# Performance work log

Measured on AMD Instinct MI355X. Metric: run time of the kernel, lower is better.

## Reference

```python
import jax, jax.numpy as jnp
import numpy as np
from jax import lax

D_INNER = 1024
D_STATE = 16
DT_RANK = 32


def conv2d(x, w, b, pad=1):
    y = lax.conv_general_dilated(x, w, (1, 1), [(pad, pad), (pad, pad)],
                                 dimension_numbers=('NCHW', 'OIHW', 'NCHW'))
    return y + b[None, :, None, None]


def maxpool2(x):
    return lax.reduce_window(x, -jnp.inf, lax.max, (1, 1, 2, 2), (1, 1, 2, 2), 'VALID')


def layer_norm(x, w, b, eps=1e-5):
    m = x.mean(-1, keepdims=True)
    v = ((x - m) ** 2).mean(-1, keepdims=True)
    return (x - m) * lax.rsqrt(v + eps) * w + b


def cblock(h, w1, b1, w2, b2):
    return jax.nn.relu(conv2d(jax.nn.relu(conv2d(h, w1, b1)), w2, b2))


def up2(d, w, b):
    # ConvTranspose2d(kernel=2, stride=2): each input pixel -> 2x2 output block
    Bn, Ci, H, W = d.shape
    y = jnp.einsum('bcij,copq->boipjq', d, w).reshape(Bn, w.shape[1], 2 * H, 2 * W)
    return y + b[None, :, None, None]


def eblock(e, d, upw, upb, w1, b1, w2, b2):
    d = up2(d, upw, upb)
    dy = e.shape[2] - d.shape[2]
    dx = e.shape[3] - d.shape[3]
    e = e[:, :, dy // 2:e.shape[2] - dy // 2, dx // 2:e.shape[3] - dx // 2]
    return cblock(jnp.concatenate([e, d], 1), w1, b1, w2, b2)


def mamba(hs, inW, cw, cb, xpW, dtW, dtB, Alog, Dp, outW):
    # standard Mamba-1 mixer: in_proj -> causal depthwise conv -> selective scan -> gate -> out_proj
    Bn, L, _ = hs.shape
    xz = jnp.einsum('bld,ed->ble', hs, inW)                       # [B,L,2*d_inner]
    xi, z = xz[..., :D_INNER], xz[..., D_INNER:]
    xc = lax.conv_general_dilated(xi.transpose(0, 2, 1), cw[:, None, :], (1,), [(3, 0)],
                                  dimension_numbers=('NCH', 'OIH', 'NCH'),
                                  feature_group_count=D_INNER)    # causal, len L
    xc = jax.nn.silu(xc + cb[None, :, None]).transpose(0, 2, 1)   # [B,L,d_inner]
    xdbl = jnp.einsum('bld,ed->ble', xc, xpW)                     # [B,L,dt_rank+2*d_state]
    dt = jax.nn.softplus(jnp.einsum('blr,dr->bld', xdbl[..., :DT_RANK], dtW) + dtB)
    Bs = xdbl[..., DT_RANK:DT_RANK + D_STATE]
    Cs = xdbl[..., DT_RANK + D_STATE:]
    A = -jnp.exp(Alog)                                            # [d_inner,d_state]
    dA = jnp.exp(dt[..., None] * A)                               # [B,L,d_inner,d_state]
    dBu = (dt * xc)[..., None] * Bs[:, :, None, :]

    def step(h, inp):
        dA_t, dBu_t, C_t = inp
        h = dA_t * h + dBu_t
        return h, jnp.einsum('bdn,bn->bd', h, C_t)

    h0 = jnp.zeros((Bn, D_INNER, D_STATE), hs.dtype)
    _, ys = lax.scan(step, h0, (dA.transpose(1, 0, 2, 3), dBu.transpose(1, 0, 2, 3), Cs.transpose(1, 0, 2)))
    y = ys.transpose(1, 0, 2) + Dp * xc
    return jnp.einsum('ble,de->bld', y * jax.nn.silu(z), outW)


def setup_inputs() -> dict:
    key = jax.random.key(0)
    ks = iter(jax.random.split(key, 80))

    def w(shape, fan_in):
        return jax.random.normal(next(ks), shape, jnp.float32) * np.float32(np.sqrt(2.0 / fan_in))

    H = W = 128
    fy = np.fft.fftfreq(H)
    fx = np.fft.fftfreq(W)
    r = np.sqrt(fy[:, None] ** 2 + fx[None, :] ** 2)
    r = r / r.max()
    bands = [(0.0, 0.15), (0.15, 0.35), (0.35, 1.0001)]
    freq_masks = jnp.asarray(np.stack([((r >= lo) & (r < hi)).astype(np.float32) for lo, hi in bands]))

    d = {}
    d['x'] = jax.random.normal(next(ks), (2, 1, H, W), jnp.float32)
    d['freq_masks'] = freq_masks
    for ci, co, n in [(3, 64, 'e1'), (64, 128, 'e2'), (128, 256, 'e3'), (256, 512, 'e4')]:
        d[n + 'w1'] = w((co, ci, 3, 3), ci * 9)
        d[n + 'b1'] = jnp.zeros((co,), jnp.float32)
        d[n + 'w2'] = w((co, co, 3, 3), co * 9)
        d[n + 'b2'] = jnp.zeros((co,), jnp.float32)
    d['cls_token'] = jnp.zeros((1, 1, 512), jnp.float32)
    d['norm_w'] = jnp.ones((24, 512), jnp.float32)
    d['norm_b'] = jnp.zeros((24, 512), jnp.float32)
    d['in_proj_w'] = w((24, 2048, 512), 512)
    d['conv1d_w'] = w((24, 1024, 4), 4)
    d['conv1d_b'] = jnp.zeros((24, 1024), jnp.float32)
    d['x_proj_w'] = w((24, 64, 1024), 1024)
    d['dt_w'] = w((24, 1024, 32), 32)
    d['dt_b'] = jnp.full((24, 1024), float(np.log(np.expm1(0.01))), jnp.float32)
    d['A_log'] = jnp.broadcast_to(jnp.log(jnp.arange(1, 17, dtype=jnp.float32)), (24, 1024, 16)) + 0.0
    d['D_ssm'] = jnp.ones((24, 1024), jnp.float32)
    d['out_proj_w'] = w((24, 512, 1024), 1024)
    for n, ci, co, cc in [('d4', 512, 256, 768), ('d3', 256, 128, 384), ('d2', 128, 64, 192), ('d1', 64, 32, 96)]:
        d[n + 'up_w'] = w((ci, co, 2, 2), ci * 4)
        d[n + 'up_b'] = jnp.zeros((co,), jnp.float32)
        d[n + 'w1'] = w((co, cc, 3, 3), cc * 9)
        d[n + 'b1'] = jnp.zeros((co,), jnp.float32)
        d[n + 'w2'] = w((co, co, 3, 3), co * 9)
        d[n + 'b2'] = jnp.zeros((co,), jnp.float32)
    d['final_w'] = w((4, 32, 1, 1), 32)
    d['final_b'] = jnp.zeros((4,), jnp.float32)
    return d


def reference(x, freq_masks, e1w1, e1b1, e1w2, e1b2, e2w1, e2b1, e2w2, e2b2,
              e3w1, e3b1, e3w2, e3b2, e4w1, e4b1, e4w2, e4b2, cls_token,
              norm_w, norm_b, in_proj_w, conv1d_w, conv1d_b, x_proj_w, dt_w, dt_b,
              A_log, D_ssm, out_proj_w,
              d4up_w, d4up_b, d4w1, d4b1, d4w2, d4b2,
              d3up_w, d3up_b, d3w1, d3b1, d3w2, d3b2,
              d2up_w, d2up_b, d2w1, d2b1, d2w2, d2b2,
              d1up_w, d1up_b, d1w1, d1b1, d1w2, d1b2,
              final_w, final_b):
    # DCT/FFT frequency split: [B,1,H,W] -> [B,3,H,W]
    xf = jnp.fft.fft2(x)
    x_freq = jnp.real(jnp.fft.ifft2(xf * freq_masks[None]))

    e1 = cblock(x_freq, e1w1, e1b1, e1w2, e1b2); p1 = maxpool2(e1)
    e2 = cblock(p1, e2w1, e2b1, e2w2, e2b2); p2 = maxpool2(e2)
    e3 = cblock(p2, e3w1, e3b1, e3w2, e3b2); p3 = maxpool2(e3)
    e4 = cblock(p3, e4w1, e4b1, e4w2, e4b2); p4 = maxpool2(e4)   # [B,512,H/16,W/16]

    Bn, _, Hs, Ws = p4.shape
    seq = p4.reshape(Bn, 512, Hs * Ws).transpose(0, 2, 1)
    tok = jnp.concatenate([jnp.broadcast_to(cls_token, (Bn, 1, 512)), seq], 1)

    params = (norm_w, norm_b, in_proj_w, conv1d_w, conv1d_b, x_proj_w, dt_w, dt_b, A_log, D_ssm, out_proj_w)

    def layer(carry, p):
        hidden, residual = carry
        nw, nb, inW, cw, cb, xpW, dtW, dtB, Alog, Dp, outW = p
        residual = residual + hidden   # first block: residual starts == hidden (faithful)
        hs = layer_norm(residual, nw, nb)
        hs = mamba(hs, inW, cw, cb, xpW, dtW, dtB, Alog, Dp, outW)
        return (hs, residual), None

    (hidden, _), _ = lax.scan(layer, (tok, tok), params)

    xsp = hidden[:, 1:, :].transpose(0, 2, 1).reshape(Bn, 512, Hs, Ws)

    d4 = eblock(e4, xsp, d4up_w, d4up_b, d4w1, d4b1, d4w2, d4b2)
    d3 = eblock(e3, d4, d3up_w, d3up_b, d3w1, d3b1, d3w2, d3b2)
    d2 = eblock(e2, d3, d2up_w, d2up_b, d2w1, d2b1, d2w2, d2b2)
    d1 = eblock(e1, d2, d1up_w, d1up_b, d1w1, d1b1, d1w2, d1b2)

    out = conv2d(d1, final_w, final_b, pad=0)
    out = jax.image.resize(out, (out.shape[0], out.shape[1], out.shape[2] * 16, out.shape[3] * 16), 'bilinear')
    return out
```

## Files before the change

kernel.cpp:

```cpp
#include <hip/hip_runtime.h>
#include <math.h>

#define PI_F 3.14159265358979323846f
typedef _Float16 f16;
typedef __attribute__((ext_vector_type(8))) _Float16 f16x8;
typedef __attribute__((ext_vector_type(4))) float f32x4;

__device__ __forceinline__ float siluf(float x){ return x / (1.f + expf(-x)); }
__device__ __forceinline__ float softplusf(float x){ return fmaxf(x,0.f) + log1pf(expf(-fabsf(x))); }
__device__ __forceinline__ void f2hl(float v, f16& hi, f16& lo){
  hi = (f16)v;
  lo = (f16)(v - (float)hi);
}

__global__ void k_dft_rows(const float* __restrict__ x, float* __restrict__ Tre, float* __restrict__ Tim){
  int v = threadIdx.x; int y = blockIdx.x; int b = blockIdx.y;
  __shared__ float cs[128], sn[128];
  float ang = -2.f*PI_F*(float)v/128.f;
  cs[v]=cosf(ang); sn[v]=sinf(ang);
  __syncthreads();
  const float* row = x + (b*128+y)*128;
  float re=0.f, im=0.f;
  for(int n=0;n<128;n++){ float xv=row[n]; int ph=(v*n)&127; re=fmaf(xv,cs[ph],re); im=fmaf(xv,sn[ph],im); }
  int o=(b*128+y)*128+v; Tre[o]=re; Tim[o]=im;
// ... 45 lines not shown
  }
  xf[((b*3+m)*128+y)*128+xc] = re*(1.f/128.f);
}

#define NWD 20
struct WAll {
  const float* src[NWD];
  int N[NWD], Kp[NWD], up[NWD], ci[NWD], cip[NWD];
  int cum[NWD+1];
};
__global__ void k_wcvt_all(WAll d, int total, f16* __restrict__ bh, f16* __restrict__ bl){
  int gid = blockIdx.x*256 + threadIdx.x;
  if (gid >= total) return;
  int li = gid; const float* src = d.src[0];
  int N=d.N[0], Kp=d.Kp[0], up=d.up[0], Ci=d.ci[0], cip=d.cip[0];
  #pragma unroll
  for (int j=1;j<NWD;j++){
    if (gid >= d.cum[j]){
      li = gid - d.cum[j]; src=d.src[j]; N=d.N[j];Kp=d.Kp[j];up=d.up[j];Ci=d.ci[j];cip=d.cip[j];
    }
  }
  int n = li / Kp, k = li - n*Kp;
  float v = 0.f;
  if (up){
    int o = n>>2, p=(n>>1)&1, q=n&1;
    if (k < Ci) v = src[(((size_t)k*up + o)*2 + p)*2 + q];
  } else {
    int tap = k / cip, cc = k - tap*cip;
    if (n < N && cc < Ci) v = src[((size_t)n*Ci + cc)*9 + tap];
  }
  f16 h,l; f2hl(v,h,l);
  bh[gid]=h; bl[gid]=l;
}

__global__ void k_im2col(const float* __restrict__ in1, int C1,
                         int H, int W, int wsh, int hwsh, int K, int Kp,
                         f16* __restrict__ Ah, f16* __restrict__ Al){
  int k = blockIdx.x*256 + threadIdx.x;
  int lm = blockIdx.y;
  if (k >= Kp) return;
  float val = 0.f;
  if (k < K){
    int m = lm;
    int b = m >> hwsh;
    int hw = m & ((1<<hwsh)-1);
    int y = hw >> wsh;
    int x = hw & (W-1);
    val = in1[(((size_t)b*C1 + k)*H + y)*W + x];
  }
  f16 h,l; f2hl(val,h,l);
  Ah[(size_t)lm*Kp + k] = h; Al[(size_t)lm*Kp + k] = l;
}

#define GLLDS(gp, ls) __builtin_amdgcn_global_load_lds( \
    (const __attribute__((address_space(1))) void*)(gp), \
    (__attribute__((address_space(3))) void*)(ls), 16, 0, 0)

template<int NL>
__global__ __launch_bounds__(256) void k_conv_ig(
    const float* __restrict__ in1, int C1, const float* __restrict__ in2, int C2,
    const f16* __restrict__ Wh, const f16* __restrict__ Wl,
    const float* __restrict__ bias, float* __restrict__ out,
    int Co, int H, int W, int wsh, int hwsh, int Cip, int civ,
    int nslabR, float* __restrict__ part, int Np)
{
  __shared__ __align__(16) float smI[2*6464];
  __shared__ __align__(16) f16 smW[3*2*2048];
  const int HW = 1<<hwsh;
  const int tw = (W<64)?W:64;
  const int twsh = (wsh<6)?wsh:6;
  const int R = 64>>twsh;
  const int RT = R+2, TWD = tw+2;
  const int nspat = RT*TWD;
  const int CS = ((nspat+3)&~3)+2;
  const int total = nspat*32;
  const int nsteps = 9*nslabR;
  const int Kp = 9*Cip;
  int slab0 = blockIdx.z*nslabR;
  int slabEnd = slab0 + nslabR;

  int bn = blockIdx.y*64;
  int bm = blockIdx.x*64;
  int t = threadIdx.x;
  int lane = t&63, wv = t>>6;
  int wr = wv>>1, wc = wv&1;

  int b  = bm >> hwsh;
  int hw0 = bm & (HW-1);
  int y0 = hw0 >> wsh;
  int x0 = hw0 & (W-1);

  float bv[2][4];
  if (!part){
    int cb = bn + wr*32 + (lane>>4)*4;
    #pragma unroll
    for (int ri=0;ri<2;ri++)
      #pragma unroll
      for (int r=0;r<4;r++){
        int co = cb + ri*16 + r;
        bv[ri][r] = bias[co < Co ? co : Co-1];
      }
    asm volatile("s_waitcnt vmcnt(0)" ::: "memory");
  }

  int goff[NL], loff[NL];
  {
    int ci = 0, s = t;
    if (s >= nspat){ s -= nspat; ci++; }
    if (s >= nspat){ s -= nspat; ci++; }
    #pragma unroll
    for (int j=0;j<NL;j++){
      int rr_=0, sx=s;
      #pragma unroll
      for (int q=0;q<5;q++){ if (sx>=TWD){ sx-=TWD; rr_++; } }
      int gy = y0 - 1 + rr_;
      int gx = x0 - 1 + sx;
      int idx = t + j*256;
      bool intile = (idx < total);
      bool ok = intile && (ci < civ) && (gy>=0) && (gy<H) && (gx>=0) && (gx<W);
      goff[j] = ok ? (ci*HW + gy*W + gx) : -1;
      loff[j] = intile ? (ci*CS + rr_*TWD + sx) : -1;
      s += 256;
      if (s >= nspat){ s -= nspat; ci++; }
      if (s >= nspat){ s -= nspat; ci++; }
      if (s >= nspat){ s -= nspat; ci++; }
    }
  }

  int rr = lane >> 2;
  int cg = (lane & 3) ^ ((lane >> 3) & 3);
  size_t gW = (size_t)(bn + wv*16 + rr)*Kp + cg*8;
  int lb = wv*512;
  auto stage = [&](int bfi, int k0){
    GLLDS(Wh + gW + k0, &smW[(bfi*2+0)*2048 + lb]);
    GLLDS(Wl + gW + k0, &smW[(bfi*2+1)*2048 + lb]);
  };

  int rA = lane & 15, c = lane >> 4;
  int RW = wr*32 + rA; int sW = (RW>>1)&3;
  int offW = RW*32 + 8*(c ^ sW);
  int lp0 = wc*32 + rA, lp1 = lp0 + 16;
  int sid0 = ((lp0>>twsh)+1)*TWD + (lp0 & (tw-1)) + 1;
  int sid1 = ((lp1>>twsh)+1)*TWD + (lp1 & (tw-1)) + 1;
  int cbase = c*8*CS;
  int csj[8];
  #pragma unroll
  for (int j=0;j<8;j++) csj[j] = j*CS;

  auto srcptr = [&](int sl) -> const float* {
    int cbeg = sl*32;
    return (cbeg < C1) ? in1 + ((size_t)(b*C1 + cbeg))*HW
                       : in2 + ((size_t)(b*C2 + (cbeg - C1)))*HW;
  };

  float rin[NL];
  {
    const float* sp = srcptr(slab0);
    #pragma unroll
    for (int j=0;j<NL;j++) rin[j] = sp[goff[j] < 0 ? 0 : goff[j]];
  }
  stage(0, 0*Cip + slab0*32);
  stage(1, 1*Cip + slab0*32);
  stage(2, 2*Cip + slab0*32);
  asm volatile("s_waitcnt vmcnt(6)" ::: "memory");
  #pragma unroll
  for (int j=0;j<NL;j++) if (loff[j] >= 0) smI[loff[j]] = (goff[j] < 0) ? 0.f : rin[j];
  asm volatile("s_waitcnt lgkmcnt(0)" ::: "memory");
  __builtin_amdgcn_s_barrier();
  asm volatile("" ::: "memory");
  if (slab0 + 1 < slabEnd){
    const float* sp = srcptr(slab0+1);
    #pragma unroll
    for (int j=0;j<NL;j++) rin[j] = sp[goff[j] < 0 ? 0 : goff[j]];
  }

  f32x4 zz = {0.f,0.f,0.f,0.f};
  f32x4 acc[2][2];
  acc[0][0]=zz; acc[0][1]=zz; acc[1][0]=zz; acc[1][1]=zz;

  int tcur = 0, scur = slab0;
  int stp_t3 = 3, stp_s3 = slab0;
  int bfi = 0;

  for (int step = 0; step < nsteps; ++step){
    if (tcur == 0 && step > 0){
      asm volatile("s_waitcnt vmcnt(6)" ::: "memory");
      int wb = ((scur - slab0) & 1)*6464;
      #pragma unroll
      for (int j=0;j<NL;j++) if (loff[j] >= 0) smI[wb + loff[j]] = (goff[j] < 0) ? 0.f : rin[j];
      asm volatile("s_waitcnt lgkmcnt(0)" ::: "memory");
      __builtin_amdgcn_s_barrier();
      asm volatile("" ::: "memory");
      if (scur + 1 < slabEnd){
        const float* sp = srcptr(scur+1);
        #pragma unroll
        for (int j=0;j<NL;j++) rin[j] = sp[goff[j] < 0 ? 0 : goff[j]];
      }
    }
    if (tcur < 3 && (scur + 1 < slabEnd)){
      if constexpr (NL == 25) asm volatile("s_waitcnt vmcnt(29)" ::: "memory");
      else if constexpr (NL == 17) asm volatile("s_waitcnt vmcnt(21)" ::: "memory");
      else asm volatile("s_waitcnt vmcnt(18)" ::: "memory");
    } else {
      asm volatile("s_waitcnt vmcnt(4)" ::: "memory");
    }
    __builtin_amdgcn_s_barrier();
    asm volatile("" ::: "memory");

    const f16* bW = &smW[bfi*4096];
    f16x8 w0h = *(const f16x8*)&bW[offW];
    f16x8 w1h = *(const f16x8*)&bW[offW + 512];
    f16x8 w0l = *(const f16x8*)&bW[2048 + offW];
    f16x8 w1l = *(const f16x8*)&bW[2048 + offW + 512];

    int t3v = (tcur >= 6) ? 2 : ((tcur >= 3) ? 1 : 0);
    int doff = (t3v - 1)*TWD + (tcur - 3*t3v) - 1;
    int ib = ((scur - slab0) & 1)*6464 + cbase;
    f16x8 p0h, p0l, p1h, p1l;
    #pragma unroll
    for (int j=0;j<8;j++){
      float v0 = smI[ib + csj[j] + sid0 + doff];
      float v1 = smI[ib + csj[j] + sid1 + doff];
      f16 h0 = (f16)v0; p0h[j] = h0; p0l[j] = (f16)(v0 - (float)h0);
      f16 h1 = (f16)v1; p1h[j] = h1; p1l[j] = (f16)(v1 - (float)h1);
    }
    acc[0][0] = __builtin_amdgcn_mfma_f32_16x16x32_f16(w0h, p0h, acc[0][0], 0,0,0);
    acc[0][1] = __builtin_amdgcn_mfma_f32_16x16x32_f16(w0h, p1h, acc[0][1], 0,0,0);
    acc[1][0] = __builtin_amdgcn_mfma_f32_16x16x32_f16(w1h, p0h, acc[1][0], 0,0,0);
    acc[1][1] = __builtin_amdgcn_mfma_f32_16x16x32_f16(w1h, p1h, acc[1][1], 0,0,0);
    acc[0][0] = __builtin_amdgcn_mfma_f32_16x16x32_f16(w0h, p0l, acc[0][0], 0,0,0);
    acc[0][1] = __builtin_amdgcn_mfma_f32_16x16x32_f16(w0h, p1l, acc[0][1], 0,0,0);
    acc[1][0] = __builtin_amdgcn_mfma_f32_16x16x32_f16(w1h, p0l, acc[1][0], 0,0,0);
    acc[1][1] = __builtin_amdgcn_mfma_f32_16x16x32_f16(w1h, p1l, acc[1][1], 0,0,0);
    acc[0][0] = __builtin_amdgcn_mfma_f32_16x16x32_f16(w0l, p0h, acc[0][0], 0,0,0);
    acc[0][1] = __builtin_amdgcn_mfma_f32_16x16x32_f16(w0l, p1h, acc[0][1], 0,0,0);
    acc[1][0] = __builtin_amdgcn_mfma_f32_16x16x32_f16(w1l, p0h, acc[1][0], 0,0,0);
    acc[1][1] = __builtin_amdgcn_mfma_f32_16x16x32_f16(w1l, p1h, acc[1][1], 0,0,0);

    __builtin_amdgcn_s_barrier();
    asm volatile("" ::: "memory");
    int k0 = (stp_s3 < slabEnd) ? (stp_t3*Cip + stp_s3*32) : (slab0*32);
    stage(bfi, k0);
    if (++stp_t3 == 9){ stp_t3 = 0; stp_s3++; }
    bfi = (bfi == 2) ? 0 : bfi + 1;
    if (++tcur == 9){ tcur = 0; scur++; }
  }

  int Mtot = gridDim.x*64;
  #pragma unroll
  for (int ri=0;ri<2;ri++)
  #pragma unroll
  for (int fc=0;fc<2;fc++)
  #pragma unroll
  for (int r=0;r<4;r++){
    int co = bn + wr*32 + ri*16 + (lane>>4)*4 + r;
    int pm = bm + wc*32 + fc*16 + (lane&15);
    if (part){
      part[((size_t)blockIdx.z*Mtot + bm + pm)*Np + co] = acc[ri][fc][r];
    } else if (co < Co){
      float v = acc[ri][fc][r] + bv[ri][r];
      v = fmaxf(v, 0.f);
      int hw = pm & (HW-1);
      out[((size_t)b*Co + co)*HW + hw] = v;
    }
  }
}

__global__ void k_creduce(const float* __restrict__ part, const float* __restrict__ bias,
                          float* __restrict__ out, int M, int Np, int msh, int cosh, int hwsh, int S){
  int i = blockIdx.x*256 + threadIdx.x;
  int Co = 1<<cosh;
  if (i >= M*Co) return;
  int co = i >> msh, m = i & (M-1);
  float v = bias[co];
  for (int s=0;s<S;s++) v += part[((size_t)s*M + m)*Np + co];
  v = fmaxf(v, 0.f);
  int HW = 1<<hwsh;
  int b = m >> hwsh, hw = m & (HW-1);
  out[((size_t)b*Co + co)*HW + hw] = v;
}

__global__ __launch_bounds__(256) void k_gemm_hl(
    const f16* __restrict__ Wh, const f16* __restrict__ Wl,
    const f16* __restrict__ Ph, const f16* __restrict__ Pl,
    const float* __restrict__ bias, float* __restrict__ out,
    int N, int Kp, int wsh, int hwsh, int Co)
{
  __shared__ __align__(16) f16 sm[3*4*2048];
  int bn = blockIdx.y*64;
  int bm = blockIdx.x*64;
  int t = threadIdx.x;
  int lane = t & 63, wv = t >> 6;
  int wr = wv >> 1, wc = wv & 1;

  float bv[2][4];
  {
    int cb = bn + wr*32 + (lane>>4)*4;
    #pragma unroll
    for (int ri=0;ri<2;ri++)
      #pragma unroll
      for (int r=0;r<4;r++){
        int co = cb + ri*16 + r;
        int idx = co>>2, lim = N>>2;
        if (idx >= lim) idx = lim-1;
        bv[ri][r] = bias[idx];
      }
  }
  asm volatile("s_waitcnt vmcnt(0)" ::: "memory");

  int rr = lane >> 2;
  int cg = (lane & 3) ^ ((lane >> 3) & 3);
  size_t gW = (size_t)(bn + wv*16 + rr)*Kp + cg*8;
// ... 29 lines not shown
    int bfi = tt % 3;
    int base = bfi*8192;
    f16x8 w0h = *(const f16x8*)&sm[base + offW];
    f16x8 w1h = *(const f16x8*)&sm[base + offW + 512];
    f16x8 w0l = *(const f16x8*)&sm[base + 2048 + offW];
    f16x8 w1l = *(const f16x8*)&sm[base + 2048 + offW + 512];
    f16x8 p0h = *(const f16x8*)&sm[base + 4096 + offP];
    f16x8 p1h = *(const f16x8*)&sm[base + 4096 + offP + 512];
    f16x8 p0l = *(const f16x8*)&sm[base + 6144 + offP];
    f16x8 p1l = *(const f16x8*)&sm[base + 6144 + offP + 512];
    acc[0][0] = __builtin_amdgcn_mfma_f32_16x16x32_f16(w0h, p0h, acc[0][0], 0,0,0);
    acc[0][1] = __builtin_amdgcn_mfma_f32_16x16x32_f16(w0h, p1h, acc[0][1], 0,0,0);
    acc[1][0] = __builtin_amdgcn_mfma_f32_16x16x32_f16(w1h, p0h, acc[1][0], 0,0,0);
    acc[1][1] = __builtin_amdgcn_mfma_f32_16x16x32_f16(w1h, p1h, acc[1][1], 0,0,0);
    acc[0][0] = __builtin_amdgcn_mfma_f32_16x16x32_f16(w0h, p0l, acc[0][0], 0,0,0);
    acc[0][1] = __builtin_amdgcn_mfma_f32_16x16x32_f16(w0h, p1l, acc[0][1], 0,0,0);
    acc[1][0] = __builtin_amdgcn_mfma_f32_16x16x32_f16(w1h, p0l, acc[1][0], 0,0,0);
    acc[1][1] = __builtin_amdgcn_mfma_f32_16x16x32_f16(w1h, p1l, acc[1][1], 0,0,0);
    acc[0][0] = __builtin_amdgcn_mfma_f32_16x16x32_f16(w0l, p0h, acc[0][0], 0,0,0);
    acc[0][1] = __builtin_amdgcn_mfma_f32_16x16x32_f16(w0l, p1h, acc[0][1], 0,0,0);
    acc[1][0] = __builtin_amdgcn_mfma_f32_16x16x32_f16(w1l, p0h, acc[1][0], 0,0,0);
    acc[1][1] = __builtin_amdgcn_mfma_f32_16x16x32_f16(w1l, p1h, acc[1][1], 0,0,0);
    __builtin_amdgcn_s_barrier();
    asm volatile("" ::: "memory");
    int kn = (tt+3 < nt) ? (tt+3)*32 : 0;
    stage(bfi, kn);
  }

  int HW = 1<<hwsh;
  int Wi = 1<<wsh;
  int Hi = 1<<(hwsh-wsh);
  #pragma unroll
  for (int ri=0;ri<2;ri++)
  #pragma unroll
  for (int fc=0;fc<2;fc++)
  #pragma unroll
  for (int r=0;r<4;r++){
    int co = bn + wr*32 + ri*16 + (lane>>4)*4 + r;
    int m = bm + wc*32 + fc*16 + (lane&15);
    if (co < N){
      int o = co>>2, p=(co>>1)&1, q=co&1;
      float v = acc[ri][fc][r] + bv[ri][r];
      int bb = m >> hwsh;
      int ij = m & (HW-1);
      int i = ij >> wsh, j = ij & (Wi-1);
      out[(((size_t)bb*Co + o)*(2*Hi) + 2*i+p)*(2*Wi) + 2*j+q] = v;
    }
  }
}

__global__ __launch_bounds__(256) void k_gemm_w32s(
    const float* __restrict__ Wf, int ldaW,
    const float* __restrict__ Pf, int ldaP,
    float* __restrict__ out, int N, int KS, int Mreal, int ldc)
{
  __shared__ __align__(16) float smW[3*2048];
  __shared__ __align__(16) float smP[3*2048];
  int bn = blockIdx.y*64;
  int bm = blockIdx.x*64;
  int kz = blockIdx.z*KS;
  int t = threadIdx.x;
  int lane = t & 63, wv = t >> 6;
  int wr = wv >> 1, wc = wv & 1;

  int wcs = (lane & 7) ^ (lane >> 3);
  size_t gWoff = (size_t)(bn + wv*16 + (lane>>3))*ldaW + wcs*4 + kz;
  size_t gPoff = (size_t)(bm + wv*16 + (lane>>3))*ldaP + wcs*4 + kz;

  int rA = lane & 15, c = lane >> 4;
  int RW0 = wr*32 + rA;  int swzW = RW0 & 7;
  int RP0 = wc*32 + rA;  int swzP = RP0 & 7;
  int cw0 = ((2*c)   ^ swzW)*4;
  int cw1 = ((2*c+1) ^ swzW)*4;
  int pc0 = ((2*c)   ^ swzP)*4;
  int pc1 = ((2*c+1) ^ swzP)*4;

  f32x4 zz = {0.f,0.f,0.f,0.f};
  f32x4 acc[2][2];
  acc[0][0]=zz; acc[0][1]=zz; acc[1][0]=zz; acc[1][1]=zz;

  auto stage = [&](int bfi, int kk){
    GLLDS(Wf + gWoff + kk,                  &smW[bfi*2048 + wv*512]);
    GLLDS(Wf + gWoff + kk + 8*(size_t)ldaW, &smW[bfi*2048 + wv*512 + 256]);
    GLLDS(Pf + gPoff + kk,                  &smP[bfi*2048 + wv*512]);
    GLLDS(Pf + gPoff + kk + 8*(size_t)ldaP, &smP[bfi*2048 + wv*512 + 256]);
  };

  int nt = KS >> 5;
  stage(0, 0);
  stage(1, (nt>1)?32:0);
  stage(2, (nt>2)?64:0);

  for (int tt = 0; tt < nt; ++tt){
    asm volatile("s_waitcnt vmcnt(8)" ::: "memory");
    __builtin_amdgcn_s_barrier();
    asm volatile("" ::: "memory");
    int bfi = tt % 3;
    const float* bW = &smW[bfi*2048];
    const float* bP = &smP[bfi*2048];
    f32x4 a0 = *(const f32x4*)&bW[RW0*32 + cw0];
    f32x4 a1 = *(const f32x4*)&bW[RW0*32 + cw1];
    f32x4 a2 = *(const f32x4*)&bW[RW0*32 + 512 + cw0];
    f32x4 a3 = *(const f32x4*)&bW[RW0*32 + 512 + cw1];
    f32x4 b0 = *(const f32x4*)&bP[RP0*32 + pc0];
    f32x4 b1 = *(const f32x4*)&bP[RP0*32 + pc1];
    f32x4 b2 = *(const f32x4*)&bP[RP0*32 + 512 + pc0];
    f32x4 b3 = *(const f32x4*)&bP[RP0*32 + 512 + pc1];
    f16x8 w0h, w0l, w1h, w1l, p0h, p0l, p1h, p1l;
    #pragma unroll
    for (int j=0;j<4;j++){
      f16 h;
      h=(f16)a0[j]; w0h[j]=h;   w0l[j]  =(f16)(a0[j]-(float)h);
      h=(f16)a1[j]; w0h[4+j]=h; w0l[4+j]=(f16)(a1[j]-(float)h);
      h=(f16)a2[j]; w1h[j]=h;   w1l[j]  =(f16)(a2[j]-(float)h);
      h=(f16)a3[j]; w1h[4+j]=h; w1l[4+j]=(f16)(a3[j]-(float)h);
      h=(f16)b0[j]; p0h[j]=h;   p0l[j]  =(f16)(b0[j]-(float)h);
      h=(f16)b1[j]; p0h[4+j]=h; p0l[4+j]=(f16)(b1[j]-(float)h);
      h=(f16)b2[j]; p1h[j]=h;   p1l[j]  =(f16)(b2[j]-(float)h);
      h=(f16)b3[j]; p1h[4+j]=h; p1l[4+j]=(f16)(b3[j]-(float)h);
    }
    acc[0][0] = __builtin_amdgcn_mfma_f32_16x16x32_f16(w0h, p0h, acc[0][0], 0,0,0);
    acc[0][1] = __builtin_amdgcn_mfma_f32_16x16x32_f16(w0h, p1h, acc[0][1], 0,0,0);
    acc[1][0] = __builtin_amdgcn_mfma_f32_16x16x32_f16(w1h, p0h, acc[1][0], 0,0,0);
    acc[1][1] = __builtin_amdgcn_mfma_f32_16x16x32_f16(w1h, p1h, acc[1][1], 0,0,0);
    acc[0][0] = __builtin_amdgcn_mfma_f32_16x16x32_f16(w0h, p0l, acc[0][0], 0,0,0);
    acc[0][1] = __builtin_amdgcn_mfma_f32_16x16x32_f16(w0h, p1l, acc[0][1], 0,0,0);
    acc[1][0] = __builtin_amdgcn_mfma_f32_16x16x32_f16(w1h, p0l, acc[1][0], 0,0,0);
    acc[1][1] = __builtin_amdgcn_mfma_f32_16x16x32_f16(w1h, p1l, acc[1][1], 0,0,0);
    acc[0][0] = __builtin_amdgcn_mfma_f32_16x16x32_f16(w0l, p0h, acc[0][0], 0,0,0);
    acc[0][1] = __builtin_amdgcn_mfma_f32_16x16x32_f16(w0l, p1h, acc[0][1], 0,0,0);
    acc[1][0] = __builtin_amdgcn_mfma_f32_16x16x32_f16(w1l, p0h, acc[1][0], 0,0,0);
    acc[1][1] = __builtin_amdgcn_mfma_f32_16x16x32_f16(w1l, p1h, acc[1][1], 0,0,0);
    __builtin_amdgcn_s_barrier();
    asm volatile("" ::: "memory");
    int kn = (tt+3 < nt) ? (tt+3)*32 : 0;
    stage(bfi, kn);
  }

  #pragma unroll
  for (int ri=0;ri<2;ri++)
  #pragma unroll
  for (int fc=0;fc<2;fc++)
  #pragma unroll
  for (int r=0;r<4;r++){
    int co = bn + wr*32 + ri*16 + (lane>>4)*4 + r;
    int m  = bm + wc*32 + fc*16 + (lane&15);
    if (m < Mreal)
      out[((size_t)blockIdx.z*192 + m)*ldc + co] = acc[ri][fc][r];
  }
}

__global__ __launch_bounds__(256) void k_dt(
    const float* __restrict__ xdp, const float* __restrict__ dtW,
    const float* __restrict__ dtB, float* __restrict__ dtb)
{
  __shared__ float smP[64*36];
  __shared__ float smW[64*36];
  int bn = blockIdx.x*64;
  int bm = blockIdx.y*64;
  int t = threadIdx.x, lane = t&63, wv = t>>6, wr = wv>>1, wc = wv&1;
  {
    int row = t>>2, c0 = (t&3)*8;
    #pragma unroll
    for (int j=0;j<8;j++){
      int cc = c0+j;
      float pv = 0.f;
      #pragma unroll
      for (int s=0;s<4;s++) pv += xdp[((size_t)(s*192) + bm+row)*64 + cc];
      smP[row*36 + cc] = pv;
      smW[row*36 + cc] = dtW[(size_t)(bn+row)*32 + cc];
    }
  }
  __syncthreads();
  int rA = lane&15, c = lane>>4;
  int c8 = c*8;
  f32x4 a0 = *(const f32x4*)&smW[(wr*32+rA)*36 + c8];
  f32x4 a1 = *(const f32x4*)&smW[(wr*32+rA)*36 + c8+4];
  f32x4 a2 = *(const f32x4*)&smW[(wr*32+16+rA)*36 + c8];
  f32x4 a3 = *(const f32x4*)&smW[(wr*32+16+rA)*36 + c8+4];
  f32x4 b0 = *(const f32x4*)&smP[(wc*32+rA)*36 + c8];
  f32x4 b1 = *(const f32x4*)&smP[(wc*32+rA)*36 + c8+4];
  f32x4 b2 = *(const f32x4*)&smP[(wc*32+16+rA)*36 + c8];
  f32x4 b3 = *(const f32x4*)&smP[(wc*32+16+rA)*36 + c8+4];
  f16x8 w0h, w0l, w1h, w1l, p0h, p0l, p1h, p1l;
  #pragma unroll
  for (int j=0;j<4;j++){
    f16 h;
    h=(f16)a0[j]; w0h[j]=h;   w0l[j]  =(f16)(a0[j]-(float)h);
    h=(f16)a1[j]; w0h[4+j]=h; w0l[4+j]=(f16)(a1[j]-(float)h);
    h=(f16)a2[j]; w1h[j]=h;   w1l[j]  =(f16)(a2[j]-(float)h);
    h=(f16)a3[j]; w1h[4+j]=h; w1l[4+j]=(f16)(a3[j]-(float)h);
    h=(f16)b0[j]; p0h[j]=h;   p0l[j]  =(f16)(b0[j]-(float)h);
    h=(f16)b1[j]; p0h[4+j]=h; p0l[4+j]=(f16)(b1[j]-(float)h);
    h=(f16)b2[j]; p1h[j]=h;   p1l[j]  =(f16)(b2[j]-(float)h);
    h=(f16)b3[j]; p1h[4+j]=h; p1l[4+j]=(f16)(b3[j]-(float)h);
  }
  f32x4 zz = {0.f,0.f,0.f,0.f};
  f32x4 acc[2][2];
  acc[0][0]=zz; acc[0][1]=zz; acc[1][0]=zz; acc[1][1]=zz;
  acc[0][0] = __builtin_amdgcn_mfma_f32_16x16x32_f16(w0h, p0h, acc[0][0], 0,0,0);
  acc[0][1] = __builtin_amdgcn_mfma_f32_16x16x32_f16(w0h, p1h, acc[0][1], 0,0,0);
// ... 197 lines not shown
  float* Fre = alloc(32768);  float* Fim = alloc(32768);
  float* Gre = alloc(196608); float* Gim = alloc(196608);
  float* xfreq = alloc(98304);
  float* tmpA = alloc(2097152);
  float* e1 = alloc(2097152);
  float* p1 = alloc(524288);
  float* e2 = alloc(1048576);
  float* p2 = alloc(262144);
  float* e3 = alloc(524288);
  float* p3 = alloc(131072);
  float* e4 = alloc(262144);
  float* p4 = alloc(65536);
  float* residual = alloc(66560);
  float* xsp = alloc(65536);
  float* tmpB = alloc(1048576);
  float* d4 = alloc(131072);
  float* d3 = alloc(262144);
  float* d2 = alloc(524288);
  float* d1 = alloc(1048576);
  float* fin = alloc(131072);
  (void)ws_size; (void)n_in; (void)in_sizes; (void)out_size;

  WAll wa;
  {
    const float* s[NWD] = { ew1[0], ew2[0], ew1[1], ew2[1], ew1[2], ew2[2], ew1[3], ew2[3],
                            dw1[0], dw2[0], dw1[1], dw2[1], dw1[2], dw2[2], dw1[3], dw2[3],
                            dup_w[0], dup_w[1], dup_w[2], dup_w[3] };
    const int N_[NWD]  = {64,64,128,128,256,256,512,512, 256,256,128,128,64,64,32,32, 1024,512,256,128};
    const int CI_[NWD] = {3,64,64,128,128,256,256,512, 768,256,384,128,192,64,96,32, 512,256,128,64};
    const int U_[NWD]  = {0,0,0,0,0,0,0,0, 0,0,0,0,0,0,0,0, 256,128,64,32};
    int cacc = 0;
    for (int i=0;i<NWD;i++){
      wa.src[i]=s[i]; wa.N[i]=N_[i]; wa.up[i]=U_[i]; wa.ci[i]=CI_[i];
      int cip = (CI_[i]+31)&~31;
      wa.cip[i] = cip;
      wa.Kp[i] = U_[i] ? CI_[i] : 9*cip;
      wa.cum[i]=cacc;
      int Np=(N_[i]+63)&~63;
      cacc += Np*wa.Kp[i];
    }
    wa.cum[NWD]=cacc;
  }
  int wtotal = wa.cum[NWD];

  f16* q = (f16*)d_out;
  f16* Ahi = q; q += MAX_A_ELEMS;
  f16* Alo = q; q += MAX_A_ELEMS;
  f16* Ball_h = q; q += wtotal;
  f16* Ball_l = q; q += wtotal;
  float* fb = (float*)q;
  size_t foff = 0;
  auto falloc = [&](size_t n){ float* p = fb + foff; foff += n; return p; };
  float* convpart = falloc(2097152);
  float* xzp  = falloc(2*192*2048);
  float* xdp  = falloc(4*192*64);
  float* hidp = falloc(8*192*512);
  float* hs   = falloc(192*512);
  float* xc   = falloc(192*1024);
  float* gt   = falloc(192*1024);
  float* dtb  = falloc(192*1024);

  hipLaunchKernelGGL(k_wcvt_all, dim3((wtotal+255)/256), dim3(256), 0, stream, wa, wtotal, Ball_h, Ball_l);

  hipLaunchKernelGGL(k_dft_rows, dim3(128,2), dim3(128), 0, stream, x, Tre, Tim);
  hipLaunchKernelGGL(k_dft_cols, dim3(128,2), dim3(128), 0, stream, Tre, Tim, Fre, Fim);
  hipLaunchKernelGGL(k_idft_cols, dim3(128,3,2), dim3(128), 0, stream, Fre, Fim, masks, Gre, Gim);
  hipLaunchKernelGGL(k_idft_rows, dim3(128,3,2), dim3(128), 0, stream, Gre, Gim, xfreq);

  auto ctz = [](int v){ int s=0; while(!(v&1)){v>>=1;s++;} return s; };
  auto conv_ig = [&](const float* i1,int C1,const float* i2,int C2,
                     int widx, const float* bias, float* o, int Co, int H){
    int Wd = H;
    int Ci = C1+C2, Cip = (Ci+31)&~31;
    int M = 2*H*Wd, Np = (Co+63)&~63;
    int wsh = ctz(Wd), hwsh = ctz(H*Wd);
    int civ = Ci < 32 ? Ci : 32;
    const f16* bh = Ball_h + wa.cum[widx];
    const f16* bl = Ball_l + wa.cum[widx];
    int nslab = Cip>>5;
    int S = 1;
    int nslabR = nslab / S;
    float* part = (S>1) ? convpart : nullptr;
    dim3 g(M/64, Np/64, S);
    if (Wd >= 64)
      hipLaunchKernelGGL((k_conv_ig<25>), g, dim3(256), 0, stream, i1,C1,i2,C2,bh,bl,bias,o,Co,H,Wd,wsh,hwsh,Cip,civ,nslabR,part,Np);
    else if (Wd == 32)
      hipLaunchKernelGGL((k_conv_ig<17>), g, dim3(256), 0, stream, i1,C1,i2,C2,bh,bl,bias,o,Co,H,Wd,wsh,hwsh,Cip,civ,nslabR,part,Np);
    else
      hipLaunchKernelGGL((k_conv_ig<14>), g, dim3(256), 0, stream, i1,C1,i2,C2,bh,bl,bias,o,Co,H,Wd,wsh,hwsh,Cip,civ,nslabR,part,Np);
    if (S > 1)
      hipLaunchKernelGGL(k_creduce, dim3((M*Co+255)/256), dim3(256), 0, stream,
                         convpart, bias, o, M, Np, ctz(M), ctz(Co), hwsh, S);
  };
  auto up_bf = [&](const float* in, int widx, const float* bias, float* o,
                   int Ci,int Co,int Hi){
    int Kp=Ci, N=4*Co;
    int M=2*Hi*Hi;
    int wsh=ctz(Hi), hwsh=ctz(Hi*Hi);
    const f16* bh = Ball_h + wa.cum[widx];
    const f16* bl = Ball_l + wa.cum[widx];
    hipLaunchKernelGGL(k_im2col, dim3((Kp+255)/256, M), dim3(256), 0, stream,
                       in, Ci, Hi, Hi, wsh, hwsh, Ci, Kp, Ahi, Alo);
    hipLaunchKernelGGL(k_gemm_hl, dim3(M/64, N/64), dim3(256), 0, stream,
                       bh, bl, Ahi, Alo, bias, o, N, Kp, wsh, hwsh, Co);
  };

  conv_ig(xfreq,3,  nullptr,0, 0, eb1[0], tmpA, 64, 128);
  conv_ig(tmpA,64,  nullptr,0, 1, eb2[0], e1,   64, 128);
  hipLaunchKernelGGL(k_maxpool2, dim3((2*64*64*64+255)/256), dim3(256), 0, stream, e1, p1, 2*64, 128,128);
  conv_ig(p1,64,    nullptr,0, 2, eb1[1], tmpA, 128, 64);
  conv_ig(tmpA,128, nullptr,0, 3, eb2[1], e2,   128, 64);
  hipLaunchKernelGGL(k_maxpool2, dim3((2*128*32*32+255)/256), dim3(256), 0, stream, e2, p2, 2*128, 64,64);
  conv_ig(p2,128,   nullptr,0, 4, eb1[2], tmpA, 256, 32);
  conv_ig(tmpA,256, nullptr,0, 5, eb2[2], e3,   256, 32);
  hipLaunchKernelGGL(k_maxpool2, dim3((2*256*16*16+255)/256), dim3(256), 0, stream, e3, p3, 2*256, 32,32);
  conv_ig(p3,256,   nullptr,0, 6, eb1[3], tmpA, 512, 16);
  conv_ig(tmpA,512, nullptr,0, 7, eb2[3], e4,   512, 16);
  hipLaunchKernelGGL(k_maxpool2, dim3((2*512*8*8+255)/256), dim3(256), 0, stream, e4, p4, 2*512, 16,16);

  hipLaunchKernelGGL(k_build_tok, dim3((2*65*512+255)/256), dim3(256), 0, stream, p4, cls, hidp, residual);
  for (int l=0;l<24;l++){
    const float* nw   = norm_w   + (size_t)l*512;
    const float* nb   = norm_b   + (size_t)l*512;
    const float* inW  = in_proj  + (size_t)l*2048*512;
    const float* cw   = conv1d_w + (size_t)l*1024*4;
    const float* cb   = conv1d_b + (size_t)l*1024;
    const float* xpW  = x_proj   + (size_t)l*64*1024;
    const float* dtW  = dt_w     + (size_t)l*1024*32;
    const float* dtB  = dt_b     + (size_t)l*1024;
    const float* Alg  = A_log    + (size_t)l*1024*16;
    const float* Dp   = D_ssm    + (size_t)l*1024;
    const float* outW = out_proj + (size_t)l*512*1024;

    hipLaunchKernelGGL(k_add_ln, dim3(130), dim3(256), 0, stream, residual, hidp, nw, nb, hs);
    hipLaunchKernelGGL(k_gemm_w32s, dim3(3,32,2), dim3(256), 0, stream,
                       inW, 512, hs, 512, xzp, 2048, 256, 130, 2048);
    hipLaunchKernelGGL(k_conv1d_silu, dim3(4,65,2), dim3(256), 0, stream, xzp, cw, cb, xc);
    hipLaunchKernelGGL(k_gemm_w32s, dim3(3,1,4), dim3(256), 0, stream,
                       xpW, 1024, xc, 1024, xdp, 64, 256, 130, 64);
    hipLaunchKernelGGL(k_dt, dim3(16,3), dim3(256), 0, stream, xdp, dtW, dtB, dtb);
    hipLaunchKernelGGL(k_scan, dim3(128), dim3(256), 0, stream, dtb, xc, xdp, xzp, Alg, Dp, gt);
    hipLaunchKernelGGL(k_gemm_w32s, dim3(3,8,8), dim3(256), 0, stream,
                       outW, 1024, gt, 1024, hidp, 512, 128, 130, 512);
  }
  hipLaunchKernelGGL(k_xsp, dim3((2*512*64+255)/256), dim3(256), 0, stream, hidp, xsp);

  up_bf(xsp, 16, dup_b[0], tmpB, 512, 256, 8);
  conv_ig(e4,512, tmpB,256, 8, db1[0], tmpA, 256, 16);
  conv_ig(tmpA,256, nullptr,0, 9, db2[0], d4, 256, 16);
  up_bf(d4, 17, dup_b[1], tmpB, 256, 128, 16);
  conv_ig(e3,256, tmpB,128, 10, db1[1], tmpA, 128, 32);
  conv_ig(tmpA,128, nullptr,0, 11, db2[1], d3, 128, 32);
  up_bf(d3, 18, dup_b[2], tmpB, 128, 64, 32);
  conv_ig(e2,128, tmpB,64, 12, db1[2], tmpA, 64, 64);
  conv_ig(tmpA,64, nullptr,0, 13, db2[2], d2, 64, 64);
  up_bf(d2, 19, dup_b[3], tmpB, 64, 32, 64);
  conv_ig(e1,64, tmpB,32, 14, db1[3], tmpA, 32, 128);
  conv_ig(tmpA,32, nullptr,0, 15, db2[3], d1, 32, 128);

  hipLaunchKernelGGL(k_conv1x1, dim3((16384+255)/256, 4, 2), dim3(256), 0, stream, d1, final_w, final_b, fin);
  hipLaunchKernelGGL(k_resize16, dim3((size_t)(2*4*2048*2048)/256), dim3(256), 0, stream, fin, out);
}
```

Before: 3.584 ms.

## Route low-resolution convs through explicit im2col plus split-K GEMM and reduce

The eight low-resolution 3x3 convolutions (16x16 and 32x32 maps) now use an explicit fp32 im2col buffer, the fp32 split-K GEMM kernel writing partial sums, and a reduction kernel that adds bias and applies ReLU. The implicit-GEMM kernel loses its unused split-K path, and the GEMM kernel takes a configurable slice stride. The aim is to fill the GPU on small spatial layers, where the implicit conv launches too few blocks. The cost is an extra im2col write and read, partial-sum traffic, and two extra launches per conv.

```diff
diff --git a/kernel.cpp b/kernel.cpp
--- a/kernel.cpp
+++ b/kernel.cpp
@@ -121,6 +121,27 @@
   Ah[(size_t)lm*Kp + k] = h; Al[(size_t)lm*Kp + k] = l;
 }
 
+__global__ void k_im2col32(const float* __restrict__ in1, int C1,
+                           const float* __restrict__ in2, int C2,
+                           int H, int W, int wsh, int hwsh, int K,
+                           float* __restrict__ A){
+  int k = blockIdx.x*256 + threadIdx.x;
+  int m = blockIdx.y;
+  if (k >= K) return;
+  int ci = k/9; int tt = k - ci*9;
+  int dy = tt/3 - 1, dx = tt - (tt/3)*3 - 1;
+  int b = m >> hwsh;
+  int hw = m & ((1<<hwsh)-1);
+  int y = (hw >> wsh) + dy;
+  int x = (hw & (W-1)) + dx;
+  float val = 0.f;
+  if (y >= 0 && y < H && x >= 0 && x < W){
+    val = (ci < C1) ? in1[(((size_t)b*C1 + ci)*H + y)*W + x]
+                    : in2[(((size_t)b*C2 + (ci-C1))*H + y)*W + x];
+  }
+  A[(size_t)m*K + k] = val;
+}
+
 #define GLLDS(gp, ls) __builtin_amdgcn_global_load_lds( \
     (const __attribute__((address_space(1))) void*)(gp), \
     (__attribute__((address_space(3))) void*)(ls), 16, 0, 0)
@@ -130,8 +151,7 @@
     const float* __restrict__ in1, int C1, const float* __restrict__ in2, int C2,
     const f16* __restrict__ Wh, const f16* __restrict__ Wl,
     const float* __restrict__ bias, float* __restrict__ out,
-    int Co, int H, int W, int wsh, int hwsh, int Cip, int civ,
-    int nslabR, float* __restrict__ part, int Np)
+    int Co, int H, int W, int wsh, int hwsh, int Cip, int civ)
 {
   __shared__ __align__(16) float smI[2*6464];
   __shared__ __align__(16) f16 smW[3*2*2048];
@@ -143,10 +163,9 @@
   const int nspat = RT*TWD;
   const int CS = ((nspat+3)&~3)+2;
   const int total = nspat*32;
-  const int nsteps = 9*nslabR;
+  const int nslab = Cip>>5;
+  const int nsteps = 9*nslab;
   const int Kp = 9*Cip;
-  int slab0 = blockIdx.z*nslabR;
-  int slabEnd = slab0 + nslabR;
 
   int bn = blockIdx.y*64;
   int bm = blockIdx.x*64;
@@ -160,7 +179,7 @@
   int x0 = hw0 & (W-1);
 
   float bv[2][4];
-  if (!part){
+  {
     int cb = bn + wr*32 + (lane>>4)*4;
     #pragma unroll
     for (int ri=0;ri<2;ri++)
@@ -224,21 +243,21 @@
 
   float rin[NL];
   {
-    const float* sp = srcptr(slab0);
+    const float* sp = srcptr(0);
     #pragma unroll
     for (int j=0;j<NL;j++) rin[j] = sp[goff[j] < 0 ? 0 : goff[j]];
   }
-  stage(0, 0*Cip + slab0*32);
-  stage(1, 1*Cip + slab0*32);
-  stage(2, 2*Cip + slab0*32);
+  stage(0, 0);
+  stage(1, Cip);
+  stage(2, 2*Cip);
   asm volatile("s_waitcnt vmcnt(6)" ::: "memory");
   #pragma unroll
   for (int j=0;j<NL;j++) if (loff[j] >= 0) smI[loff[j]] = (goff[j] < 0) ? 0.f : rin[j];
   asm volatile("s_waitcnt lgkmcnt(0)" ::: "memory");
   __builtin_amdgcn_s_barrier();
   asm volatile("" ::: "memory");
-  if (slab0 + 1 < slabEnd){
-    const float* sp = srcptr(slab0+1);
+  if (nslab > 1){
+    const float* sp = srcptr(1);
     #pragma unroll
     for (int j=0;j<NL;j++) rin[j] = sp[goff[j] < 0 ? 0 : goff[j]];
   }
@@ -247,26 +266,26 @@
   f32x4 acc[2][2];
   acc[0][0]=zz; acc[0][1]=zz; acc[1][0]=zz; acc[1][1]=zz;
 
-  int tcur = 0, scur = slab0;
-  int stp_t3 = 3, stp_s3 = slab0;
+  int tcur = 0, scur = 0;
+  int stp_t3 = 3, stp_s3 = 0;
   int bfi = 0;
 
   for (int step = 0; step < nsteps; ++step){
     if (tcur == 0 && step > 0){
       asm volatile("s_waitcnt vmcnt(6)" ::: "memory");
-      int wb = ((scur - slab0) & 1)*6464;
+      int wb = (scur & 1)*6464;
       #pragma unroll
       for (int j=0;j<NL;j++) if (loff[j] >= 0) smI[wb + loff[j]] = (goff[j] < 0) ? 0.f : rin[j];
       asm volatile("s_waitcnt lgkmcnt(0)" ::: "memory");
       __builtin_amdgcn_s_barrier();
       asm volatile("" ::: "memory");
-      if (scur + 1 < slabEnd){
+      if (scur + 1 < nslab){
         const float* sp = srcptr(scur+1);
         #pragma unroll
         for (int j=0;j<NL;j++) rin[j] = sp[goff[j] < 0 ? 0 : goff[j]];
       }
     }
-    if (tcur < 3 && (scur + 1 < slabEnd)){
+    if (tcur < 3 && (scur + 1 < nslab)){
       if constexpr (NL == 25) asm volatile("s_waitcnt vmcnt(29)" ::: "memory");
       else if constexpr (NL == 17) asm volatile("s_waitcnt vmcnt(21)" ::: "memory");
       else asm volatile("s_waitcnt vmcnt(18)" ::: "memory");
@@ -284,7 +303,7 @@
 
     int t3v = (tcur >= 6) ? 2 : ((tcur >= 3) ? 1 : 0);
     int doff = (t3v - 1)*TWD + (tcur - 3*t3v) - 1;
-    int ib = ((scur - slab0) & 1)*6464 + cbase;
+    int ib = (scur & 1)*6464 + cbase;
     f16x8 p0h, p0l, p1h, p1l;
     #pragma unroll
     for (int j=0;j<8;j++){
@@ -308,14 +327,13 @@
 
     __builtin_amdgcn_s_barrier();
     asm volatile("" ::: "memory");
-    int k0 = (stp_s3 < slabEnd) ? (stp_t3*Cip + stp_s3*32) : (slab0*32);
+    int k0 = (stp_s3 < nslab) ? (stp_t3*Cip + stp_s3*32) : 0;
     stage(bfi, k0);
     if (++stp_t3 == 9){ stp_t3 = 0; stp_s3++; }
     bfi = (bfi == 2) ? 0 : bfi + 1;
     if (++tcur == 9){ tcur = 0; scur++; }
   }
 
-  int Mtot = gridDim.x*64;
   #pragma unroll
   for (int ri=0;ri<2;ri++)
   #pragma unroll
@@ -324,9 +342,7 @@
   for (int r=0;r<4;r++){
     int co = bn + wr*32 + ri*16 + (lane>>4)*4 + r;
     int pm = bm + wc*32 + fc*16 + (lane&15);
-    if (part){
-      part[((size_t)blockIdx.z*Mtot + bm + pm)*Np + co] = acc[ri][fc][r];
-    } else if (co < Co){
+    if (co < Co){
       float v = acc[ri][fc][r] + bv[ri][r];
       v = fmaxf(v, 0.f);
       int hw = pm & (HW-1);
@@ -462,7 +478,7 @@
 __global__ __launch_bounds__(256) void k_gemm_w32s(
     const float* __restrict__ Wf, int ldaW,
     const float* __restrict__ Pf, int ldaP,
-    float* __restrict__ out, int N, int KS, int Mreal, int ldc)
+    float* __restrict__ out, int N, int KS, int Mreal, int ldc, int sliceStride)
 {
   __shared__ __align__(16) float smW[3*2048];
   __shared__ __align__(16) float smP[3*2048];
@@ -556,7 +572,7 @@
     int co = bn + wr*32 + ri*16 + (lane>>4)*4 + r;
     int m  = bm + wc*32 + fc*16 + (lane&15);
     if (m < Mreal)
-      out[((size_t)blockIdx.z*192 + m)*ldc + co] = acc[ri][fc][r];
+      out[((size_t)blockIdx.z*sliceStride + m)*ldc + co] = acc[ri][fc][r];
   }
 }
 
@@ -860,6 +876,7 @@
   size_t foff = 0;
   auto falloc = [&](size_t n){ float* p = fb + foff; foff += n; return p; };
   float* convpart = falloc(2097152);
+  float* Af32 = falloc(7340032);
   float* xzp  = falloc(2*192*2048);
   float* xdp  = falloc(4*192*64);
   float* hidp = falloc(8*192*512);
@@ -885,20 +902,27 @@
     int civ = Ci < 32 ? Ci : 32;
     const f16* bh = Ball_h + wa.cum[widx];
     const f16* bl = Ball_l + wa.cum[widx];
-    int nslab = Cip>>5;
-    int S = 1;
-    int nslabR = nslab / S;
-    float* part = (S>1) ? convpart : nullptr;
-    dim3 g(M/64, Np/64, S);
+    dim3 g(M/64, Np/64);
     if (Wd >= 64)
-      hipLaunchKernelGGL((k_conv_ig<25>), g, dim3(256), 0, stream, i1,C1,i2,C2,bh,bl,bias,o,Co,H,Wd,wsh,hwsh,Cip,civ,nslabR,part,Np);
+      hipLaunchKernelGGL((k_conv_ig<25>), g, dim3(256), 0, stream, i1,C1,i2,C2,bh,bl,bias,o,Co,H,Wd,wsh,hwsh,Cip,civ);
     else if (Wd == 32)
-      hipLaunchKernelGGL((k_conv_ig<17>), g, dim3(256), 0, stream, i1,C1,i2,C2,bh,bl,bias,o,Co,H,Wd,wsh,hwsh,Cip,civ,nslabR,part,Np);
+      hipLaunchKernelGGL((k_conv_ig<17>), g, dim3(256), 0, stream, i1,C1,i2,C2,bh,bl,bias,o,Co,H,Wd,wsh,hwsh,Cip,civ);
     else
-      hipLaunchKernelGGL((k_conv_ig<14>), g, dim3(256), 0, stream, i1,C1,i2,C2,bh,bl,bias,o,Co,H,Wd,wsh,hwsh,Cip,civ,nslabR,part,Np);
-    if (S > 1)
-      hipLaunchKernelGGL(k_creduce, dim3((M*Co+255)/256), dim3(256), 0, stream,
-                         convpart, bias, o, M, Np, ctz(M), ctz(Co), hwsh, S);
+      hipLaunchKernelGGL((k_conv_ig<14>), g, dim3(256), 0, stream, i1,C1,i2,C2,bh,bl,bias,o,Co,H,Wd,wsh,hwsh,Cip,civ);
+  };
+  auto conv_sk = [&](const float* i1,int C1,const float* i2,int C2,
+                     const float* wraw, const float* bias, float* o, int Co, int H, int S){
+    int Wd = H;
+    int Ci = C1+C2, K = Ci*9;
+    int M = 2*H*Wd;
+    int wsh = ctz(Wd), hwsh = ctz(H*Wd);
+    hipLaunchKernelGGL(k_im2col32, dim3((K+255)/256, M), dim3(256), 0, stream,
+                       i1, C1, i2, C2, H, Wd, wsh, hwsh, K, Af32);
+    int KS = K / S;
+    hipLaunchKernelGGL(k_gemm_w32s, dim3(M/64, Co/64, S), dim3(256), 0, stream,
+                       wraw, K, Af32, K, convpart, Co, KS, M, Co, M);
+    hipLaunchKernelGGL(k_creduce, dim3((M*Co+255)/256), dim3(256), 0, stream,
+                       convpart, bias, o, M, Co, ctz(M), ctz(Co), hwsh, S);
   };
   auto up_bf = [&](const float* in, int widx, const float* bias, float* o,
                    int Ci,int Co,int Hi){
@@ -919,11 +943,11 @@
   conv_ig(p1,64,    nullptr,0, 2, eb1[1], tmpA, 128, 64);
   conv_ig(tmpA,128, nullptr,0, 3, eb2[1], e2,   128, 64);
   hipLaunchKernelGGL(k_maxpool2, dim3((2*128*32*32+255)/256), dim3(256), 0, stream, e2, p2, 2*128, 64,64);
-  conv_ig(p2,128,   nullptr,0, 4, eb1[2], tmpA, 256, 32);
-  conv_ig(tmpA,256, nullptr,0, 5, eb2[2], e3,   256, 32);
+  conv_sk(p2,128,   nullptr,0, ew1[2], eb1[2], tmpA, 256, 32, 4);
+  conv_sk(tmpA,256, nullptr,0, ew2[2], eb2[2], e3,   256, 32, 4);
   hipLaunchKernelGGL(k_maxpool2, dim3((2*256*16*16+255)/256), dim3(256), 0, stream, e3, p3, 2*256, 32,32);
-  conv_ig(p3,256,   nullptr,0, 6, eb1[3], tmpA, 512, 16);
-  conv_ig(tmpA,512, nullptr,0, 7, eb2[3], e4,   512, 16);
+  conv_sk(p3,256,   nullptr,0, ew1[3], eb1[3], tmpA, 512, 16, 8);
+  conv_sk(tmpA,512, nullptr,0, ew2[3], eb2[3], e4,   512, 16, 8);
   hipLaunchKernelGGL(k_maxpool2, dim3((2*512*8*8+255)/256), dim3(256), 0, stream, e4, p4, 2*512, 16,16);
 
   hipLaunchKernelGGL(k_build_tok, dim3((2*65*512+255)/256), dim3(256), 0, stream, p4, cls, hidp, residual);
@@ -942,23 +966,23 @@
 
     hipLaunchKernelGGL(k_add_ln, dim3(130), dim3(256), 0, stream, residual, hidp, nw, nb, hs);
     hipLaunchKernelGGL(k_gemm_w32s, dim3(3,32,2), dim3(256), 0, stream,
-                       inW, 512, hs, 512, xzp, 2048, 256, 130, 2048);
+                       inW, 512, hs, 512, xzp, 2048, 256, 130, 2048, 192);
     hipLaunchKernelGGL(k_conv1d_silu, dim3(4,65,2), dim3(256), 0, stream, xzp, cw, cb, xc);
     hipLaunchKernelGGL(k_gemm_w32s, dim3(3,1,4), dim3(256), 0, stream,
-                       xpW, 1024, xc, 1024, xdp, 64, 256, 130, 64);
+                       xpW, 1024, xc, 1024, xdp, 64, 256, 130, 64, 192);
     hipLaunchKernelGGL(k_dt, dim3(16,3), dim3(256), 0, stream, xdp, dtW, dtB, dtb);
     hipLaunchKernelGGL(k_scan, dim3(128), dim3(256), 0, stream, dtb, xc, xdp, xzp, Alg, Dp, gt);
     hipLaunchKernelGGL(k_gemm_w32s, dim3(3,8,8), dim3(256), 0, stream,
-                       outW, 1024, gt, 1024, hidp, 512, 128, 130, 512);
+                       outW, 1024, gt, 1024, hidp, 512, 128, 130, 512, 192);
   }
   hipLaunchKernelGGL(k_xsp, dim3((2*512*64+255)/256), dim3(256), 0, stream, hidp, xsp);
 
   up_bf(xsp, 16, dup_b[0], tmpB, 512, 256, 8);
-  conv_ig(e4,512, tmpB,256, 8, db1[0], tmpA, 256, 16);
-  conv_ig(tmpA,256, nullptr,0, 9, db2[0], d4, 256, 16);
+  conv_sk(e4,512, tmpB,256, dw1[0], db1[0], tmpA, 256, 16, 8);
+  conv_sk(tmpA,256, nullptr,0, dw2[0], db2[0], d4, 256, 16, 8);
   up_bf(d4, 17, dup_b[1], tmpB, 256, 128, 16);
-  conv_ig(e3,256, tmpB,128, 10, db1[1], tmpA, 128, 32);
-  conv_ig(tmpA,128, nullptr,0, 11, db2[1], d3, 128, 32);
+  conv_sk(e3,256, tmpB,128, dw1[1], db1[1], tmpA, 128, 32, 4);
+  conv_sk(tmpA,128, nullptr,0, dw2[1], db2[1], d3, 128, 32, 4);
   up_bf(d3, 18, dup_b[2], tmpB, 128, 64, 32);
   conv_ig(e2,128, tmpB,64, 12, db1[2], tmpA, 64, 64);
   conv_ig(tmpA,64, nullptr,0, 13, db2[2], d2, 64, 64);
```

New measurement: 3.120 ms (median of 3 runs). -12.9%, faster.
